# Performance work log

Measured on AMD Instinct MI355X. Metric: run time of the kernel, lower is better.

Reference implementation:

```python
import jax, jax.numpy as jnp
import numpy as np

B, I, H = 16384, 512, 512


def _linear_params(key, out_dim, in_dim):
    kw, kb = jax.random.split(key)
    bound = 1.0 / np.sqrt(in_dim)
    W = jax.random.uniform(kw, (out_dim, in_dim), jnp.float32, -bound, bound)
    b = jax.random.uniform(kb, (out_dim,), jnp.float32, -bound, bound)
    return W, b


def setup_inputs() -> dict:
    key = jax.random.key(0)
    ks = jax.random.split(key, 12)
    x = jax.random.normal(ks[0], (B, I), jnp.float32)
    h_prev = jax.random.normal(ks[1], (B, H), jnp.float32)
    c_prev = jax.random.normal(ks[2], (B, H), jnp.float32)
    W_xi, b_xi = _linear_params(ks[3], H, I)
    W_hi, b_hi = _linear_params(ks[4], H, H)
    W_xf, b_xf = _linear_params(ks[5], H, I)
    W_hf, b_hf = _linear_params(ks[6], H, H)
    W_xc, b_xc = _linear_params(ks[7], H, I)
    W_hc, b_hc = _linear_params(ks[8], H, H)
    W_xo, b_xo = _linear_params(ks[9], H, I)
    W_ho, b_ho = _linear_params(ks[10], H, H)
    W_e, b_e = _linear_params(ks[11], H, I + H)
    return dict(x=x, h_prev=h_prev, c_prev=c_prev,
                W_xi=W_xi, b_xi=b_xi, W_hi=W_hi, b_hi=b_hi,
                W_xf=W_xf, b_xf=b_xf, W_hf=W_hf, b_hf=b_hf,
                W_xc=W_xc, b_xc=b_xc, W_hc=W_hc, b_hc=b_hc,
                W_xo=W_xo, b_xo=b_xo, W_ho=W_ho, b_ho=b_ho,
                W_e=W_e, b_e=b_e)


def reference(x, h_prev, c_prev,
              W_xi, b_xi, W_hi, b_hi,
              W_xf, b_xf, W_hf, b_hf,
              W_xc, b_xc, W_hc, b_hc,
              W_xo, b_xo, W_ho, b_ho,
              W_e, b_e):
    # Batch the 4 input-to-hidden projections into one GEMM and the 4
    # hidden-to-hidden projections into another (same math as 8 Linears).
    Wx = jnp.concatenate([W_xi, W_xf, W_xc, W_xo], axis=0)   # [4H, I]
    bx = jnp.concatenate([b_xi, b_xf, b_xc, b_xo], axis=0)   # [4H]
    Wh = jnp.concatenate([W_hi, W_hf, W_hc, W_ho], axis=0)   # [4H, H]
    bh = jnp.concatenate([b_hi, b_hf, b_hc, b_ho], axis=0)
    gates = (x @ Wx.T + bx) + (h_prev @ Wh.T + bh)            # [B, 4H]
    gi, gf, gc, go = jnp.split(gates, 4, axis=-1)
    i = jax.nn.sigmoid(gi)
    f = jax.nn.sigmoid(gf)
    g = jnp.tanh(gc)
    o = jax.nn.sigmoid(go)
    c = f * c_prev + i * g
    # exp gate: Linear on [x, h_prev] -> tanh -> exp; split W_e to avoid concat
    We_x, We_h = W_e[:, :x.shape[-1]], W_e[:, x.shape[-1]:]
    exp_factor = jnp.exp(jnp.tanh(x @ We_x.T + h_prev @ We_h.T + b_e))
    h = o * jnp.tanh(c) * exp_factor
    return (h, c)
```

## Files before the change

kernel.cpp:

```cpp
#include <hip/hip_runtime.h>
#include <stdint.h>

#define Bsz 16384
#define Hh  512
#define Kd  1024
#define BM  128
#define BNJ 32
#define BK  32
#define NT  32

#define BUFB 18432

typedef __attribute__((ext_vector_type(8))) short bf16x8;
typedef __attribute__((ext_vector_type(4))) float f32x4;
typedef __attribute__((ext_vector_type(8))) unsigned short u16x8;

__device__ __forceinline__ unsigned short f2bf(float f) {
    union { float f; unsigned u; } v; v.f = f;
    unsigned u = v.u;
    return (unsigned short)((u + 0x7fffu + ((u >> 16) & 1u)) >> 16);
}
__device__ __forceinline__ float fast_tanh(float x) {
    float e = __expf(2.f * x);
    return (e - 1.f) / (e + 1.f);
}
__device__ __forceinline__ float fast_sigmoid(float x) {
    return 1.f / (1.f + __expf(-x));
}

__global__ void pack_A(const float* __restrict__ x, const float* __restrict__ h,
                       unsigned short* __restrict__ A) {
    const long total = (long)Bsz * Kd / 8;
    for (long i = (long)blockIdx.x * blockDim.x + threadIdx.x; i < total;
         i += (long)gridDim.x * blockDim.x) {
        long row = i >> 7;
        int  col = ((int)(i & 127)) << 3;
        const float* src = (col < 512) ? (x + row * 512 + col)
                                       : (h + row * 512 + (col - 512));
        float4 f0 = *(const float4*)(src);
        float4 f1 = *(const float4*)(src + 4);
        u16x8 o;
        o[0]=f2bf(f0.x); o[1]=f2bf(f0.y); o[2]=f2bf(f0.z); o[3]=f2bf(f0.w);
        o[4]=f2bf(f1.x); o[5]=f2bf(f1.y); o[6]=f2bf(f1.z); o[7]=f2bf(f1.w);
        *(u16x8*)(A + (i << 3)) = o;
    }
}

__global__ void pack_B(const float* __restrict__ Wxi, const float* __restrict__ Whi,
                       const float* __restrict__ Wxf, const float* __restrict__ Whf,
                       const float* __restrict__ Wxc, const float* __restrict__ Whc,
                       const float* __restrict__ Wxo, const float* __restrict__ Who,
                       const float* __restrict__ We,
                       const float* __restrict__ bxi, const float* __restrict__ bhi,
                       const float* __restrict__ bxf, const float* __restrict__ bhf,
                       const float* __restrict__ bxc, const float* __restrict__ bhc,
                       const float* __restrict__ bxo, const float* __restrict__ bho,
                       const float* __restrict__ be,
                       unsigned short* __restrict__ Bp, float* __restrict__ bias) {
    const long id = (long)blockIdx.x * blockDim.x + threadIdx.x;
    if (id < 327680) {
        int blk = (int)(id >> 6);
        int l   = (int)(id & 63);
        int kh  = blk & 1;
        int kt  = (blk >> 1) & 15;
        int rest = blk >> 5;
        int g    = rest % 5;
        int jgrp = rest / 5;
        int j  = jgrp * 16 + (l & 15);
        int k0 = kt * 64 + kh * 32 + ((l >> 4) << 3);
        const float* src;
        if (g == 4) {
            src = We + (long)j * 1024 + k0;
        } else {
            const float* Wx = (g == 0) ? Wxi : (g == 1) ? Wxf : (g == 2) ? Wxc : Wxo;
            const float* Wh = (g == 0) ? Whi : (g == 1) ? Whf : (g == 2) ? Whc : Who;
            src = (k0 < 512) ? (Wx + (long)j * 512 + k0)
                             : (Wh + (long)j * 512 + (k0 - 512));
        }
        float4 f0 = *(const float4*)(src);
        float4 f1 = *(const float4*)(src + 4);
        u16x8 o;
        o[0]=f2bf(f0.x); o[1]=f2bf(f0.y); o[2]=f2bf(f0.z); o[3]=f2bf(f0.w);
        o[4]=f2bf(f1.x); o[5]=f2bf(f1.y); o[6]=f2bf(f1.z); o[7]=f2bf(f1.w);
        *(u16x8*)(Bp + (long)blk * 512 + l * 8) = o;
    }
    if (id < 2560) {
        int row = (int)id;
        int g = row >> 9, j = row & 511;
        float b;
        if (g == 4) b = be[j];
        else {
            const float* bx = (g == 0) ? bxi : (g == 1) ? bxf : (g == 2) ? bxc : bxo;
            const float* bh = (g == 0) ? bhi : (g == 1) ? bhf : (g == 2) ? bhc : bho;
            b = bx[j] + bh[j];
        }
        bias[row] = b;
    }
}

#define GL16(g, l) __builtin_amdgcn_global_load_lds( \
    (const __attribute__((address_space(1))) unsigned int*)(g), \
    (__attribute__((address_space(3))) unsigned int*)(l), 16, 0, 0)

#define VM0()      asm volatile("s_waitcnt vmcnt(0)" ::: "memory")
#define LGKM0()    asm volatile("s_waitcnt lgkmcnt(0)" ::: "memory")
#define BARRIER()  asm volatile("s_barrier" ::: "memory")
#define SCHED0()   __builtin_amdgcn_sched_barrier(0)

#define MF(a, b, c) __builtin_amdgcn_mfma_f32_16x16x32_bf16(a, b, c, 0, 0, 0)

#define RD9(RBO) do { \
    afA[0] = *(const bf16x8*)(aP + (RBO) + 0 * 1024); \
    afA[1] = *(const bf16x8*)(aP + (RBO) + 1 * 1024); \
    afA[2] = *(const bf16x8*)(aP + (RBO) + 2 * 1024); \
    afA[3] = *(const bf16x8*)(aP + (RBO) + 3 * 1024); \
    bq[0]  = *(const bf16x8*)(bP + (RBO) + 0 * 1024); \
    bq[1]  = *(const bf16x8*)(bP + (RBO) + 1 * 1024); \
    bq[2]  = *(const bf16x8*)(bP + (RBO) + 2 * 1024); \
    bq[3]  = *(const bf16x8*)(bP + (RBO) + 3 * 1024); \
    bq[4]  = *(const bf16x8*)(bP + (RBO) + 4 * 1024); \
} while (0)

#define MFMA20() do { \
    __builtin_amdgcn_s_setprio(1); \
    _Pragma("unroll") \
    for (int g_ = 0; g_ < 5; ++g_) { \
        acc[g_][0] = MF(afA[0], bq[g_], acc[g_][0]); \
        acc[g_][1] = MF(afA[1], bq[g_], acc[g_][1]); \
        acc[g_][2] = MF(afA[2], bq[g_], acc[g_][2]); \
        acc[g_][3] = MF(afA[3], bq[g_], acc[g_][3]); \
    } \
    __builtin_amdgcn_s_setprio(0); \
} while (0)

#define SG5(SO, T) do { \
    GL16(asg0 + (T) * 32,  lds_raw + (SO) + adst0); \
    GL16(asg1 + (T) * 32,  lds_raw + (SO) + adst1); \
    GL16(bsg0 + (T) * 512, lds_raw + (SO) + bdo0); \
    GL16(bsg1 + (T) * 512, lds_raw + (SO) + bdo1); \
    GL16(bsg2 + (T) * 512, lds_raw + (SO) + bdo2); \
} while (0)

#define TILE(RBO, SBO, T, STG, SYNC) do { \
    if (STG) SG5(SBO, (T) + 1); \
    RD9(RBO); \
    LGKM0(); SCHED0(); \
    MFMA20(); \
    if (SYNC) { VM0(); BARRIER(); } \
} while (0)

__global__ __launch_bounds__(256, 3)
void xlstm_gemm(const unsigned short* __restrict__ A,
                const unsigned short* __restrict__ Bp,
                const float* __restrict__ bias,
                const float* __restrict__ c_prev,
                float* __restrict__ out) {
    __shared__ __align__(16) unsigned char lds_raw[2 * BUFB];

    const int tid  = threadIdx.x;
    const int wid  = tid >> 6;
    const int lane = tid & 63;
    const int wm   = wid >> 1;
    const int wj   = wid & 1;
    const int fr   = lane & 15;
    const int q    = lane >> 4;

    const int orig = blockIdx.x;
    const int wg   = (orig & 7) * 256 + (orig >> 3);
    const int mblk = wg >> 4;
    const int jblk = wg & 15;
    const long brow = (long)mblk * BM;
    const int  bcol = jblk * BNJ;

    f32x4 acc[5][4];
#pragma unroll
    for (int g = 0; g < 5; ++g)
#pragma unroll
        for (int m = 0; m < 4; ++m)
#pragma unroll
            for (int r = 0; r < 4; ++r) acc[g][m][r] = 0.f;

    bf16x8 afA[4];
    bf16x8 bq[5];

    const unsigned char* aP = lds_raw + wm * 4096 + fr * 64
                              + ((q ^ ((fr >> 1) & 3)) << 4);
    const unsigned char* bP = lds_raw + 8192 + wj * 5120 + lane * 16;

    const int arow = tid >> 2;
    const unsigned short* asg0 = A + (brow + arow) * 1024L
                                   + (((tid & 3) ^ ((arow >> 1) & 3)) << 3);
    const unsigned short* asg1 = asg0 + 65536;
    const int adst0 = tid * 16;
    const int adst1 = tid * 16 + 4096;
    const unsigned short *bsg0, *bsg1, *bsg2;
    int bdo0, bdo1, bdo2;
#define BSTG_INIT(i) do { \
    int u_ = wid + 4 * (i); if (u_ >= 10) u_ -= 10; \
    int jl_ = u_ / 5; int g_ = u_ - 5 * jl_; \
    bsg##i = Bp + (long)(jblk * 2 + jl_) * 81920 + g_ * 16384 + lane * 8; \
    bdo##i = 8192 + u_ * 1024 + lane * 16; \
} while (0)
    BSTG_INIT(0); BSTG_INIT(1); BSTG_INIT(2);
#undef BSTG_INIT

    SG5(0, 0);
    VM0();
    BARRIER();

    for (int t = 0; t < 30; t += 2) {
        TILE(0,    BUFB, t,     1, 1);
        TILE(BUFB, 0,    t + 1, 1, 1);
    }
    TILE(0,    BUFB, 30, 1, 1);
    TILE(BUFB, 0,    31, 0, 0);

    const int j = bcol + wj * 16 + fr;
    const float bi_ = bias[j];
    const float bf_ = bias[512 + j];
    const float bc_ = bias[1024 + j];
    const float bo_ = bias[1536 + j];
    const float be_ = bias[2048 + j];
    const long mbase = brow + wm * 64 + (q << 2);
#pragma unroll
    for (int m = 0; m < 4; ++m) {
#pragma unroll
        for (int r = 0; r < 4; ++r) {
            long row = mbase + m * 16 + r;
            float gi = acc[0][m][r] + bi_;
            float gf = acc[1][m][r] + bf_;
            float gc = acc[2][m][r] + bc_;
            float go = acc[3][m][r] + bo_;
            float ge = acc[4][m][r] + be_;
            float iv = fast_sigmoid(gi);
            float fv = fast_sigmoid(gf);
            float gv = fast_tanh(gc);
            float ov = fast_sigmoid(go);
            float ef = __expf(fast_tanh(ge));
            float cp = c_prev[row * 512 + j];
            float cv = fv * cp + iv * gv;
            float hv = ov * fast_tanh(cv) * ef;
            out[row * 512 + j] = hv;
            out[(long)Bsz * 512 + row * 512 + j] = cv;
        }
    }
}

extern "C" void kernel_launch(void* const* d_in, const int* in_sizes, int n_in,
                              void* d_out, int out_size, void* d_ws, size_t ws_size,
                              hipStream_t stream) {
    const float* x      = (const float*)d_in[0];
    const float* h_prev = (const float*)d_in[1];
    const float* c_prev = (const float*)d_in[2];
    const float* Wxi = (const float*)d_in[3];
    const float* bxi = (const float*)d_in[4];
    const float* Whi = (const float*)d_in[5];
    const float* bhi = (const float*)d_in[6];
    const float* Wxf = (const float*)d_in[7];
    const float* bxf = (const float*)d_in[8];
    const float* Whf = (const float*)d_in[9];
    const float* bhf = (const float*)d_in[10];
    const float* Wxc = (const float*)d_in[11];
    const float* bxc = (const float*)d_in[12];
    const float* Whc = (const float*)d_in[13];
    const float* bhc = (const float*)d_in[14];
    const float* Wxo = (const float*)d_in[15];
    const float* bxo = (const float*)d_in[16];
    const float* Who = (const float*)d_in[17];
    const float* bho = (const float*)d_in[18];
    const float* We  = (const float*)d_in[19];
    const float* be  = (const float*)d_in[20];

    unsigned short* Abf  = (unsigned short*)d_ws;
    unsigned short* Bp   = (unsigned short*)((char*)d_ws + 33554432);
    float*          bias = (float*)((char*)d_ws + 33554432 + 5242880);

    pack_A<<<2048, 256, 0, stream>>>(x, h_prev, Abf);
    pack_B<<<1280, 256, 0, stream>>>(Wxi, Whi, Wxf, Whf, Wxc, Whc, Wxo, Who, We,
                                     bxi, bhi, bxf, bhf, bxc, bhc, bxo, bho, be,
                                     Bp, bias);
    xlstm_gemm<<<2048, 256, 0, stream>>>(Abf, Bp, bias, c_prev, (float*)d_out);
}
```

Before: 121.2 us.

## Triple-buffer A tiles with partial vmcnt waits for deeper prefetch

```diff
diff --git a/kernel.cpp b/kernel.cpp
--- a/kernel.cpp
+++ b/kernel.cpp
@@ -9,7 +9,7 @@
 #define BK  32
 #define NT  32
 
-#define BUFB 18432
+#define BBASE 24576
 
 typedef __attribute__((ext_vector_type(8))) short bf16x8;
 typedef __attribute__((ext_vector_type(4))) float f32x4;
@@ -102,23 +102,24 @@
     (const __attribute__((address_space(1))) unsigned int*)(g), \
     (__attribute__((address_space(3))) unsigned int*)(l), 16, 0, 0)
 
-#define VM0()      asm volatile("s_waitcnt vmcnt(0)" ::: "memory")
+#define VM_I(n)    asm volatile("s_waitcnt vmcnt(" #n ")" ::: "memory")
+#define VM(n)      VM_I(n)
 #define LGKM0()    asm volatile("s_waitcnt lgkmcnt(0)" ::: "memory")
 #define BARRIER()  asm volatile("s_barrier" ::: "memory")
 #define SCHED0()   __builtin_amdgcn_sched_barrier(0)
 
 #define MF(a, b, c) __builtin_amdgcn_mfma_f32_16x16x32_bf16(a, b, c, 0, 0, 0)
 
-#define RD9(RBO) do { \
-    afA[0] = *(const bf16x8*)(aP + (RBO) + 0 * 1024); \
-    afA[1] = *(const bf16x8*)(aP + (RBO) + 1 * 1024); \
-    afA[2] = *(const bf16x8*)(aP + (RBO) + 2 * 1024); \
-    afA[3] = *(const bf16x8*)(aP + (RBO) + 3 * 1024); \
-    bq[0]  = *(const bf16x8*)(bP + (RBO) + 0 * 1024); \
-    bq[1]  = *(const bf16x8*)(bP + (RBO) + 1 * 1024); \
-    bq[2]  = *(const bf16x8*)(bP + (RBO) + 2 * 1024); \
-    bq[3]  = *(const bf16x8*)(bP + (RBO) + 3 * 1024); \
-    bq[4]  = *(const bf16x8*)(bP + (RBO) + 4 * 1024); \
+#define RD9(ABO, BBO) do { \
+    afA[0] = *(const bf16x8*)(aP + (ABO) + 0 * 1024); \
+    afA[1] = *(const bf16x8*)(aP + (ABO) + 1 * 1024); \
+    afA[2] = *(const bf16x8*)(aP + (ABO) + 2 * 1024); \
+    afA[3] = *(const bf16x8*)(aP + (ABO) + 3 * 1024); \
+    bq[0]  = *(const bf16x8*)(bP + (BBO) + 0 * 1024); \
+    bq[1]  = *(const bf16x8*)(bP + (BBO) + 1 * 1024); \
+    bq[2]  = *(const bf16x8*)(bP + (BBO) + 2 * 1024); \
+    bq[3]  = *(const bf16x8*)(bP + (BBO) + 3 * 1024); \
+    bq[4]  = *(const bf16x8*)(bP + (BBO) + 4 * 1024); \
 } while (0)
 
 #define MFMA20() do { \
@@ -133,20 +134,24 @@
     __builtin_amdgcn_s_setprio(0); \
 } while (0)
 
-#define SG5(SO, T) do { \
-    GL16(asg0 + (T) * 32,  lds_raw + (SO) + adst0); \
-    GL16(asg1 + (T) * 32,  lds_raw + (SO) + adst1); \
-    GL16(bsg0 + (T) * 512, lds_raw + (SO) + bdo0); \
-    GL16(bsg1 + (T) * 512, lds_raw + (SO) + bdo1); \
-    GL16(bsg2 + (T) * 512, lds_raw + (SO) + bdo2); \
-} while (0)
-
-#define TILE(RBO, SBO, T, STG, SYNC) do { \
-    if (STG) SG5(SBO, (T) + 1); \
-    RD9(RBO); \
+#define SGA2(SAO, T) do { \
+    GL16(asg0 + (T) * 32, lds_raw + (SAO) + adst0); \
+    GL16(asg1 + (T) * 32, lds_raw + (SAO) + adst1); \
+} while (0)
+
+#define SGB3(SBO, T) do { \
+    GL16(bsg0 + (T) * 512, lds_raw + BBASE + (SBO) + bdo0); \
+    GL16(bsg1 + (T) * 512, lds_raw + BBASE + (SBO) + bdo1); \
+    GL16(bsg2 + (T) * 512, lds_raw + BBASE + (SBO) + bdo2); \
+} while (0)
+
+#define TILE(ABO, BBO, SAO, SBO, T, SA, SB, WN, SYNC) do { \
+    RD9(ABO, BBO); \
+    if (SB) SGB3(SBO, (T) + 1); \
+    if (SA) SGA2(SAO, (T) + 2); \
     LGKM0(); SCHED0(); \
     MFMA20(); \
-    if (SYNC) { VM0(); BARRIER(); } \
+    if (SYNC) { VM(WN); BARRIER(); } \
 } while (0)
 
 __global__ __launch_bounds__(256, 3)
@@ -155,7 +160,7 @@
                 const float* __restrict__ bias,
                 const float* __restrict__ c_prev,
                 float* __restrict__ out) {
-    __shared__ __align__(16) unsigned char lds_raw[2 * BUFB];
+    __shared__ __align__(16) unsigned char lds_raw[45056];
 
     const int tid  = threadIdx.x;
     const int wid  = tid >> 6;
@@ -185,7 +190,7 @@
 
     const unsigned char* aP = lds_raw + wm * 4096 + fr * 64
                               + ((q ^ ((fr >> 1) & 3)) << 4);
-    const unsigned char* bP = lds_raw + 8192 + wj * 5120 + lane * 16;
+    const unsigned char* bP = lds_raw + BBASE + wj * 5120 + lane * 16;
 
     const int arow = tid >> 2;
     const unsigned short* asg0 = A + (brow + arow) * 1024L
@@ -199,21 +204,27 @@
     int u_ = wid + 4 * (i); if (u_ >= 10) u_ -= 10; \
     int jl_ = u_ / 5; int g_ = u_ - 5 * jl_; \
     bsg##i = Bp + (long)(jblk * 2 + jl_) * 81920 + g_ * 16384 + lane * 8; \
-    bdo##i = 8192 + u_ * 1024 + lane * 16; \
+    bdo##i = u_ * 1024 + lane * 16; \
 } while (0)
     BSTG_INIT(0); BSTG_INIT(1); BSTG_INIT(2);
 #undef BSTG_INIT
 
-    SG5(0, 0);
-    VM0();
+    SGB3(0, 0);
+    SGA2(0, 0);
+    SGA2(8192, 1);
+    VM(2);
     BARRIER();
 
-    for (int t = 0; t < 30; t += 2) {
-        TILE(0,    BUFB, t,     1, 1);
-        TILE(BUFB, 0,    t + 1, 1, 1);
-    }
-    TILE(0,    BUFB, 30, 1, 1);
-    TILE(BUFB, 0,    31, 0, 0);
+    for (int t = 0; t < 30; t += 6) {
+        TILE(0,     0,     16384, 10240, t + 0, 1, 1, 2, 1);
+        TILE(8192,  10240, 0,     0,     t + 1, 1, 1, 2, 1);
+        TILE(16384, 0,     8192,  10240, t + 2, 1, 1, 2, 1);
+        TILE(0,     10240, 16384, 0,     t + 3, 1, 1, 2, 1);
+        TILE(8192,  0,     0,     10240, t + 4, 1, 1, 2, 1);
+        TILE(16384, 10240, 8192,  0,     t + 5, 1, 1, 2, 1);
+    }
+    TILE(0,    0,     0, 10240, 30, 0, 1, 0, 1);
+    TILE(8192, 10240, 0, 0,     31, 0, 0, 0, 0);
 
     const int j = bcol + wj * 16 + fr;
     const float bi_ = bias[j];
```

Result: no change. 119.3 us (-1.5%).

## Enlarge GEMM tile to 256 rows, BK 64, with triple-buffered LDS pipeline

Applied to the files above, without the earlier changes.

```diff
diff --git a/kernel.cpp b/kernel.cpp
--- a/kernel.cpp
+++ b/kernel.cpp
@@ -4,12 +4,12 @@
 #define Bsz 16384
 #define Hh  512
 #define Kd  1024
-#define BM  128
+#define BM  256
 #define BNJ 32
-#define BK  32
-#define NT  32
-
-#define BUFB 18432
+#define BK  64
+#define NT  16
+
+#define BUFB 53248
 
 typedef __attribute__((ext_vector_type(8))) short bf16x8;
 typedef __attribute__((ext_vector_type(4))) float f32x4;
@@ -102,60 +102,69 @@
     (const __attribute__((address_space(1))) unsigned int*)(g), \
     (__attribute__((address_space(3))) unsigned int*)(l), 16, 0, 0)
 
-#define VM0()      asm volatile("s_waitcnt vmcnt(0)" ::: "memory")
+#define VM_I(n)    asm volatile("s_waitcnt vmcnt(" #n ")" ::: "memory")
+#define VM(n)      VM_I(n)
 #define LGKM0()    asm volatile("s_waitcnt lgkmcnt(0)" ::: "memory")
 #define BARRIER()  asm volatile("s_barrier" ::: "memory")
 #define SCHED0()   __builtin_amdgcn_sched_barrier(0)
 
 #define MF(a, b, c) __builtin_amdgcn_mfma_f32_16x16x32_bf16(a, b, c, 0, 0, 0)
 
-#define RD9(RBO) do { \
-    afA[0] = *(const bf16x8*)(aP + (RBO) + 0 * 1024); \
-    afA[1] = *(const bf16x8*)(aP + (RBO) + 1 * 1024); \
-    afA[2] = *(const bf16x8*)(aP + (RBO) + 2 * 1024); \
-    afA[3] = *(const bf16x8*)(aP + (RBO) + 3 * 1024); \
-    bq[0]  = *(const bf16x8*)(bP + (RBO) + 0 * 1024); \
-    bq[1]  = *(const bf16x8*)(bP + (RBO) + 1 * 1024); \
-    bq[2]  = *(const bf16x8*)(bP + (RBO) + 2 * 1024); \
-    bq[3]  = *(const bf16x8*)(bP + (RBO) + 3 * 1024); \
-    bq[4]  = *(const bf16x8*)(bP + (RBO) + 4 * 1024); \
+#define RDPH(RBO, APK) do { \
+    af[0] = *(const bf16x8*)(APK + (RBO) + 0 * 2048); \
+    af[1] = *(const bf16x8*)(APK + (RBO) + 1 * 2048); \
+    af[2] = *(const bf16x8*)(APK + (RBO) + 2 * 2048); \
+    af[3] = *(const bf16x8*)(APK + (RBO) + 3 * 2048); \
+} while (0)
+#define RDB5(RBO, KH) do { \
+    bq[0] = *(const bf16x8*)(bP + (RBO) + (0 + (KH)) * 1024); \
+    bq[1] = *(const bf16x8*)(bP + (RBO) + (2 + (KH)) * 1024); \
+    bq[2] = *(const bf16x8*)(bP + (RBO) + (4 + (KH)) * 1024); \
+    bq[3] = *(const bf16x8*)(bP + (RBO) + (6 + (KH)) * 1024); \
+    bq[4] = *(const bf16x8*)(bP + (RBO) + (8 + (KH)) * 1024); \
 } while (0)
 
 #define MFMA20() do { \
     __builtin_amdgcn_s_setprio(1); \
     _Pragma("unroll") \
     for (int g_ = 0; g_ < 5; ++g_) { \
-        acc[g_][0] = MF(afA[0], bq[g_], acc[g_][0]); \
-        acc[g_][1] = MF(afA[1], bq[g_], acc[g_][1]); \
-        acc[g_][2] = MF(afA[2], bq[g_], acc[g_][2]); \
-        acc[g_][3] = MF(afA[3], bq[g_], acc[g_][3]); \
+        acc[g_][0] = MF(af[0], bq[g_], acc[g_][0]); \
+        acc[g_][1] = MF(af[1], bq[g_], acc[g_][1]); \
+        acc[g_][2] = MF(af[2], bq[g_], acc[g_][2]); \
+        acc[g_][3] = MF(af[3], bq[g_], acc[g_][3]); \
     } \
     __builtin_amdgcn_s_setprio(0); \
 } while (0)
 
-#define SG5(SO, T) do { \
-    GL16(asg0 + (T) * 32,  lds_raw + (SO) + adst0); \
-    GL16(asg1 + (T) * 32,  lds_raw + (SO) + adst1); \
-    GL16(bsg0 + (T) * 512, lds_raw + (SO) + bdo0); \
-    GL16(bsg1 + (T) * 512, lds_raw + (SO) + bdo1); \
-    GL16(bsg2 + (T) * 512, lds_raw + (SO) + bdo2); \
-} while (0)
-
-#define TILE(RBO, SBO, T, STG, SYNC) do { \
-    if (STG) SG5(SBO, (T) + 1); \
-    RD9(RBO); \
+#define GLA(SBO, T, I) GL16(asg + (I) * 65536 + (T) * 64, \
+                            lds_raw + (SBO) + adst + (I) * 8192)
+#define GLB(SBO, T, I) GL16(bsg##I + (T) * 1024, lds_raw + (SBO) + bdo##I)
+
+#define TILE(RBO, SBO, T, STG, VMF, WN) do { \
+     \
+    RDPH(RBO, aPk0); RDB5(RBO, 0); \
+    if (STG) { GLA(SBO, (T)+2, 0); GLA(SBO, (T)+2, 1); GLB(SBO, (T)+2, 0); } \
+    BARRIER(); \
     LGKM0(); SCHED0(); \
     MFMA20(); \
-    if (SYNC) { VM0(); BARRIER(); } \
-} while (0)
-
-__global__ __launch_bounds__(256, 3)
+    BARRIER(); \
+     \
+    RDPH(RBO, aPk1); RDB5(RBO, 1); \
+    if (STG) { GLA(SBO, (T)+2, 2); GLA(SBO, (T)+2, 3); GLB(SBO, (T)+2, 1); GLB(SBO, (T)+2, 2); } \
+    BARRIER(); \
+    LGKM0(); SCHED0(); \
+    MFMA20(); \
+    if (VMF) VM(WN); \
+    BARRIER(); \
+} while (0)
+
+__global__ __launch_bounds__(512, 2)
 void xlstm_gemm(const unsigned short* __restrict__ A,
                 const unsigned short* __restrict__ Bp,
                 const float* __restrict__ bias,
                 const float* __restrict__ c_prev,
                 float* __restrict__ out) {
-    __shared__ __align__(16) unsigned char lds_raw[2 * BUFB];
+    __shared__ __align__(16) unsigned char lds_raw[3 * BUFB];
 
     const int tid  = threadIdx.x;
     const int wid  = tid >> 6;
@@ -166,7 +175,7 @@
     const int q    = lane >> 4;
 
     const int orig = blockIdx.x;
-    const int wg   = (orig & 7) * 256 + (orig >> 3);
+    const int wg   = (orig & 7) * 128 + (orig >> 3);
     const int mblk = wg >> 4;
     const int jblk = wg & 15;
     const long brow = (long)mblk * BM;
@@ -180,40 +189,48 @@
 #pragma unroll
             for (int r = 0; r < 4; ++r) acc[g][m][r] = 0.f;
 
-    bf16x8 afA[4];
+    bf16x8 af[4];
     bf16x8 bq[5];
 
-    const unsigned char* aP = lds_raw + wm * 4096 + fr * 64
-                              + ((q ^ ((fr >> 1) & 3)) << 4);
-    const unsigned char* bP = lds_raw + 8192 + wj * 5120 + lane * 16;
-
-    const int arow = tid >> 2;
-    const unsigned short* asg0 = A + (brow + arow) * 1024L
-                                   + (((tid & 3) ^ ((arow >> 1) & 3)) << 3);
-    const unsigned short* asg1 = asg0 + 65536;
-    const int adst0 = tid * 16;
-    const int adst1 = tid * 16 + 4096;
+    const int aboff = (wm * 64 + fr) * 128;
+    const int swz0  = ((q) ^ (fr & 7)) << 4;
+    const int swz1  = ((4 | q) ^ (fr & 7)) << 4;
+    const unsigned char* aPk0 = lds_raw + aboff + swz0;
+    const unsigned char* aPk1 = lds_raw + aboff + swz1;
+    const unsigned char* bP   = lds_raw + 32768 + wj * 10240 + lane * 16;
+
+    const int r0_ = tid >> 3;
+    const unsigned short* asg = A + (brow + r0_) * 1024L
+                                  + (((tid & 7) ^ (r0_ & 7)) << 3);
+    const int adst = tid * 16;
     const unsigned short *bsg0, *bsg1, *bsg2;
     int bdo0, bdo1, bdo2;
 #define BSTG_INIT(i) do { \
-    int u_ = wid + 4 * (i); if (u_ >= 10) u_ -= 10; \
-    int jl_ = u_ / 5; int g_ = u_ - 5 * jl_; \
-    bsg##i = Bp + (long)(jblk * 2 + jl_) * 81920 + g_ * 16384 + lane * 8; \
-    bdo##i = 8192 + u_ * 1024 + lane * 16; \
+    int u_ = wid + 8 * (i); if (u_ >= 20) u_ -= 20; \
+    int jl_ = u_ / 10; int rr_ = u_ - 10 * jl_; \
+    int g_ = rr_ >> 1; int kh_ = rr_ & 1; \
+    bsg##i = Bp + (long)(jblk * 2 + jl_) * 81920 + g_ * 16384 + kh_ * 512 + lane * 8; \
+    bdo##i = 32768 + u_ * 1024 + lane * 16; \
 } while (0)
     BSTG_INIT(0); BSTG_INIT(1); BSTG_INIT(2);
 #undef BSTG_INIT
 
-    SG5(0, 0);
-    VM0();
+    GLA(0, 0, 0); GLA(0, 0, 1); GLA(0, 0, 2); GLA(0, 0, 3);
+    GLB(0, 0, 0); GLB(0, 0, 1); GLB(0, 0, 2);
+    GLA(BUFB, 1, 0); GLA(BUFB, 1, 1); GLA(BUFB, 1, 2); GLA(BUFB, 1, 3);
+    GLB(BUFB, 1, 0); GLB(BUFB, 1, 1); GLB(BUFB, 1, 2);
+    VM(7);
     BARRIER();
 
-    for (int t = 0; t < 30; t += 2) {
-        TILE(0,    BUFB, t,     1, 1);
-        TILE(BUFB, 0,    t + 1, 1, 1);
-    }
-    TILE(0,    BUFB, 30, 1, 1);
-    TILE(BUFB, 0,    31, 0, 0);
+    for (int t = 0; t < 12; t += 3) {
+        TILE(0 * BUFB, 2 * BUFB, t + 0, 1, 1, 7);
+        TILE(1 * BUFB, 0 * BUFB, t + 1, 1, 1, 7);
+        TILE(2 * BUFB, 1 * BUFB, t + 2, 1, 1, 7);
+    }
+    TILE(0 * BUFB, 2 * BUFB, 12, 1, 1, 7);
+    TILE(1 * BUFB, 0 * BUFB, 13, 1, 1, 7);
+    TILE(2 * BUFB, 0,        14, 0, 1, 0);
+    TILE(0 * BUFB, 0,        15, 0, 0, 0);
 
     const int j = bcol + wj * 16 + fr;
     const float bi_ = bias[j];
@@ -279,5 +296,5 @@
     pack_B<<<1280, 256, 0, stream>>>(Wxi, Whi, Wxf, Whf, Wxc, Whc, Wxo, Who, We,
                                      bxi, bhi, bxf, bhf, bxc, bhc, bxo, bho, be,
                                      Bp, bias);
-    xlstm_gemm<<<2048, 256, 0, stream>>>(Abf, Bp, bias, c_prev, (float*)d_out);
-}
+    xlstm_gemm<<<1024, 512, 0, stream>>>(Abf, Bp, bias, c_prev, (float*)d_out);
+}
```

Result: no change. 123.4 us (+1.9%).

## Deepen GEMM pipeline to four LDS stages with register double-buffered fragments

Applied to the files above, without the earlier changes.

```diff
diff --git a/kernel.cpp b/kernel.cpp
--- a/kernel.cpp
+++ b/kernel.cpp
@@ -9,7 +9,8 @@
 #define BK  32
 #define NT  32
 
-#define BUFB 18432
+#define AOFF(b) ((b) * 8192)
+#define BOFF(b) ((b) * 10240)
 
 typedef __attribute__((ext_vector_type(8))) short bf16x8;
 typedef __attribute__((ext_vector_type(4))) float f32x4;
@@ -102,60 +103,62 @@
     (const __attribute__((address_space(1))) unsigned int*)(g), \
     (__attribute__((address_space(3))) unsigned int*)(l), 16, 0, 0)
 
-#define VM0()      asm volatile("s_waitcnt vmcnt(0)" ::: "memory")
-#define LGKM0()    asm volatile("s_waitcnt lgkmcnt(0)" ::: "memory")
+#define VM_I(n)    asm volatile("s_waitcnt vmcnt(" #n ")" ::: "memory")
+#define VM(n)      VM_I(n)
+#define LGKM_I(n)  asm volatile("s_waitcnt lgkmcnt(" #n ")" ::: "memory")
+#define LGKM(n)    LGKM_I(n)
 #define BARRIER()  asm volatile("s_barrier" ::: "memory")
 #define SCHED0()   __builtin_amdgcn_sched_barrier(0)
 
 #define MF(a, b, c) __builtin_amdgcn_mfma_f32_16x16x32_bf16(a, b, c, 0, 0, 0)
 
-#define RD9(RBO) do { \
-    afA[0] = *(const bf16x8*)(aP + (RBO) + 0 * 1024); \
-    afA[1] = *(const bf16x8*)(aP + (RBO) + 1 * 1024); \
-    afA[2] = *(const bf16x8*)(aP + (RBO) + 2 * 1024); \
-    afA[3] = *(const bf16x8*)(aP + (RBO) + 3 * 1024); \
-    bq[0]  = *(const bf16x8*)(bP + (RBO) + 0 * 1024); \
-    bq[1]  = *(const bf16x8*)(bP + (RBO) + 1 * 1024); \
-    bq[2]  = *(const bf16x8*)(bP + (RBO) + 2 * 1024); \
-    bq[3]  = *(const bf16x8*)(bP + (RBO) + 3 * 1024); \
-    bq[4]  = *(const bf16x8*)(bP + (RBO) + 4 * 1024); \
-} while (0)
-
-#define MFMA20() do { \
+#define RD9(S, RB) do { \
+    a##S##0 = *(const bf16x8*)(aRP + AOFF(RB) + 0 * 1024); \
+    a##S##1 = *(const bf16x8*)(aRP + AOFF(RB) + 1 * 1024); \
+    a##S##2 = *(const bf16x8*)(aRP + AOFF(RB) + 2 * 1024); \
+    a##S##3 = *(const bf16x8*)(aRP + AOFF(RB) + 3 * 1024); \
+    b##S##0 = *(const bf16x8*)(bRP + BOFF(RB) + 0 * 1024); \
+    b##S##1 = *(const bf16x8*)(bRP + BOFF(RB) + 1 * 1024); \
+    b##S##2 = *(const bf16x8*)(bRP + BOFF(RB) + 2 * 1024); \
+    b##S##3 = *(const bf16x8*)(bRP + BOFF(RB) + 3 * 1024); \
+    b##S##4 = *(const bf16x8*)(bRP + BOFF(RB) + 4 * 1024); \
+} while (0)
+
+#define MF4(S, G) \
+    acc[G][0] = MF(a##S##0, b##S##G, acc[G][0]); \
+    acc[G][1] = MF(a##S##1, b##S##G, acc[G][1]); \
+    acc[G][2] = MF(a##S##2, b##S##G, acc[G][2]); \
+    acc[G][3] = MF(a##S##3, b##S##G, acc[G][3]);
+
+#define MFMA20(S) do { \
     __builtin_amdgcn_s_setprio(1); \
-    _Pragma("unroll") \
-    for (int g_ = 0; g_ < 5; ++g_) { \
-        acc[g_][0] = MF(afA[0], bq[g_], acc[g_][0]); \
-        acc[g_][1] = MF(afA[1], bq[g_], acc[g_][1]); \
-        acc[g_][2] = MF(afA[2], bq[g_], acc[g_][2]); \
-        acc[g_][3] = MF(afA[3], bq[g_], acc[g_][3]); \
-    } \
+    MF4(S, 0) MF4(S, 1) MF4(S, 2) MF4(S, 3) MF4(S, 4) \
     __builtin_amdgcn_s_setprio(0); \
 } while (0)
 
-#define SG5(SO, T) do { \
-    GL16(asg0 + (T) * 32,  lds_raw + (SO) + adst0); \
-    GL16(asg1 + (T) * 32,  lds_raw + (SO) + adst1); \
-    GL16(bsg0 + (T) * 512, lds_raw + (SO) + bdo0); \
-    GL16(bsg1 + (T) * 512, lds_raw + (SO) + bdo1); \
-    GL16(bsg2 + (T) * 512, lds_raw + (SO) + bdo2); \
-} while (0)
-
-#define TILE(RBO, SBO, T, STG, SYNC) do { \
-    if (STG) SG5(SBO, (T) + 1); \
-    RD9(RBO); \
-    LGKM0(); SCHED0(); \
-    MFMA20(); \
-    if (SYNC) { VM0(); BARRIER(); } \
-} while (0)
-
-__global__ __launch_bounds__(256, 3)
+#define SG5(SB, T) do { \
+    GL16(asg0 + (T) * 32,  lds_raw + AOFF(SB) + adst0); \
+    GL16(asg1 + (T) * 32,  lds_raw + AOFF(SB) + adst1); \
+    GL16(bsg0 + (T) * 512, lds_raw + 32768 + BOFF(SB) + bdo0); \
+    GL16(bsg1 + (T) * 512, lds_raw + 32768 + BOFF(SB) + bdo1); \
+    GL16(bsg2 + (T) * 512, lds_raw + 32768 + BOFF(SB) + bdo2); \
+} while (0)
+
+#define STEP(SC, SN, RB, SB, T) do { \
+    SG5(SB, (T) + 3); \
+    RD9(SN, RB); \
+    LGKM(9); SCHED0(); \
+    MFMA20(SC); \
+    VM(5); BARRIER(); \
+} while (0)
+
+__global__ __launch_bounds__(256, 2)
 void xlstm_gemm(const unsigned short* __restrict__ A,
                 const unsigned short* __restrict__ Bp,
                 const float* __restrict__ bias,
                 const float* __restrict__ c_prev,
                 float* __restrict__ out) {
-    __shared__ __align__(16) unsigned char lds_raw[2 * BUFB];
+    __shared__ __align__(16) unsigned char lds_raw[73728];
 
     const int tid  = threadIdx.x;
     const int wid  = tid >> 6;
@@ -180,12 +183,12 @@
 #pragma unroll
             for (int r = 0; r < 4; ++r) acc[g][m][r] = 0.f;
 
-    bf16x8 afA[4];
-    bf16x8 bq[5];
-
-    const unsigned char* aP = lds_raw + wm * 4096 + fr * 64
-                              + ((q ^ ((fr >> 1) & 3)) << 4);
-    const unsigned char* bP = lds_raw + 8192 + wj * 5120 + lane * 16;
+    bf16x8 aP0, aP1, aP2, aP3, bP0, bP1, bP2, bP3, bP4;
+    bf16x8 aQ0, aQ1, aQ2, aQ3, bQ0, bQ1, bQ2, bQ3, bQ4;
+
+    const unsigned char* aRP = lds_raw + wm * 4096 + fr * 64
+                               + ((q ^ ((fr >> 1) & 3)) << 4);
+    const unsigned char* bRP = lds_raw + 32768 + wj * 5120 + lane * 16;
 
     const int arow = tid >> 2;
     const unsigned short* asg0 = A + (brow + arow) * 1024L
@@ -199,21 +202,38 @@
     int u_ = wid + 4 * (i); if (u_ >= 10) u_ -= 10; \
     int jl_ = u_ / 5; int g_ = u_ - 5 * jl_; \
     bsg##i = Bp + (long)(jblk * 2 + jl_) * 81920 + g_ * 16384 + lane * 8; \
-    bdo##i = 8192 + u_ * 1024 + lane * 16; \
+    bdo##i = u_ * 1024 + lane * 16; \
 } while (0)
     BSTG_INIT(0); BSTG_INIT(1); BSTG_INIT(2);
 #undef BSTG_INIT
 
     SG5(0, 0);
-    VM0();
+    SG5(1, 1);
+    SG5(2, 2);
+    VM(5);
     BARRIER();
-
-    for (int t = 0; t < 30; t += 2) {
-        TILE(0,    BUFB, t,     1, 1);
-        TILE(BUFB, 0,    t + 1, 1, 1);
-    }
-    TILE(0,    BUFB, 30, 1, 1);
-    TILE(BUFB, 0,    31, 0, 0);
+    RD9(P, 0);
+
+    for (int tq = 0; tq < 28; tq += 4) {
+        STEP(P, Q, 1, 3, tq + 0);
+        STEP(Q, P, 2, 0, tq + 1);
+        STEP(P, Q, 3, 1, tq + 2);
+        STEP(Q, P, 0, 2, tq + 3);
+    }
+    SG5(3, 31);
+    RD9(Q, 1);
+    LGKM(9); SCHED0();
+    MFMA20(P);
+    VM(5); BARRIER();
+    RD9(P, 2);
+    LGKM(9); SCHED0();
+    MFMA20(Q);
+    VM(0); BARRIER();
+    RD9(Q, 3);
+    LGKM(9); SCHED0();
+    MFMA20(P);
+    LGKM(0); SCHED0();
+    MFMA20(Q);
 
     const int j = bcol + wj * 16 + fr;
     const float bi_ = bias[j];
```

Result: slower. 130.9 us (+8.1%).
